# Performance work log

Measured on AMD Instinct MI355X. Metric: run time of the kernel, lower is better.

Reference implementation:

```python
import jax, jax.numpy as jnp
import numpy as np

D_MODEL = 1024
NUM_ATOMS = 16384
TEMPERATURE = 1.0
NEG_INF = -1e9


def setup_inputs() -> dict:
    key = jax.random.key(0)
    kx, kd, km = jax.random.split(key, 3)
    x = jax.random.normal(kx, (4, 2048, D_MODEL), dtype=jnp.float32)
    # xavier_uniform for [num_atoms, d_model]
    limit = float(np.sqrt(6.0 / (NUM_ATOMS + D_MODEL)))
    dictionary = jax.random.uniform(
        kd, (NUM_ATOMS, D_MODEL), dtype=jnp.float32, minval=-limit, maxval=limit
    )
    mask = jax.random.randint(km, (4, 2048, NUM_ATOMS), 0, 2, dtype=jnp.int32)
    return {"x": x, "dictionary": dictionary, "mask": mask}


def reference(x, dictionary, mask):
    # scores: [b, s, num_atoms]
    scores = jnp.einsum("bsd,ad->bsa", x, dictionary)
    m = mask.astype(scores.dtype)
    scores = scores * m + (1.0 - m) * NEG_INF
    weights = jax.nn.softmax(scores / TEMPERATURE, axis=-1)
    reconstruction = jnp.einsum("bsa,ad->bsd", weights, dictionary)
    argmax_indices = jnp.argmax(scores, axis=-1)
    return reconstruction, argmax_indices
```

## Files before the change

kernel.cpp:

```cpp
#include <hip/hip_runtime.h>

#define NTOK   8192
#define DMODEL 1024
#define NATOM  16384

typedef _Float16 half8  __attribute__((ext_vector_type(8)));
typedef _Float16 half4_t __attribute__((ext_vector_type(4)));
typedef float    f32x4  __attribute__((ext_vector_type(4)));

#define GLOAD_LDS16(gsrc, ldst) \
  __builtin_amdgcn_global_load_lds((const __attribute__((address_space(1))) unsigned int*)(gsrc), \
                                   (__attribute__((address_space(3))) unsigned int*)(ldst), 16, 0, 0)

__global__ void cvt_f32_f16(const float* __restrict__ in, _Float16* __restrict__ out, int n4) {
  int i = blockIdx.x * 256 + threadIdx.x;
  if (i >= n4) return;
  float4 v = ((const float4*)in)[i];
  half4_t h;
  h[0] = (_Float16)v.x; h[1] = (_Float16)v.y; h[2] = (_Float16)v.z; h[3] = (_Float16)v.w;
  ((half4_t*)out)[i] = h;
}

__global__ void transpose_dict(const float* __restrict__ dict,
                               _Float16* __restrict__ Dh, _Float16* __restrict__ dT) {
  __shared__ _Float16 tile[64][68];
  int a0 = blockIdx.x * 64;
  int d0 = blockIdx.y * 64;
  int tid = threadIdx.x;
  int c = tid & 63;
  int r0 = tid >> 6;
  #pragma unroll
  for (int i = 0; i < 16; i++) {
    int r = r0 + i * 4;
    _Float16 h = (_Float16)dict[(size_t)(a0 + r) * DMODEL + d0 + c];
    tile[r][c] = h;
    Dh[(size_t)(a0 + r) * DMODEL + d0 + c] = h;
  }
  __syncthreads();
  #pragma unroll
  for (int i = 0; i < 16; i++) {
    int rd = r0 + i * 4;
    dT[(size_t)(d0 + rd) * NATOM + a0 + c] = tile[c][rd];
  }
}

__global__ void zero_lsum(float* __restrict__ lsum) {
  lsum[blockIdx.x * 256 + threadIdx.x] = 0.0f;
}

__device__ __forceinline__ void stage_ab(const _Float16* __restrict__ A,
                                         const _Float16* __restrict__ B,
                                         _Float16* As, _Float16* Bs,
                                         size_t arow0, size_t brow0, size_t ldk,
                                         int k0, int tid) {
  #pragma unroll
  for (int i = 0; i < 2; i++) {
    int L = tid + i * 256;
    int r = L >> 2, pc = L & 3;
    int c = pc ^ ((r >> 1) & 3);
    GLOAD_LDS16(A + (arow0 + r) * ldk + k0 + c * 8, As + (size_t)L * 8);
    GLOAD_LDS16(B + (brow0 + r) * ldk + k0 + c * 8, Bs + (size_t)L * 8);
  }
}

__launch_bounds__(256, 2)
__global__ void score_kernel(const _Float16* __restrict__ Xh,
                             const _Float16* __restrict__ Dh,
                             const int* __restrict__ mask,
                             _Float16* __restrict__ E,
                             float* __restrict__ lsum,
                             _Float16* __restrict__ Tmax) {
  __shared__ _Float16 lds[17408];
  const int tid  = threadIdx.x;
  const int lane = tid & 63;
  const int wave = tid >> 6;
  const int wm = wave >> 1, wn = wave & 1;
  const int m0 = blockIdx.y * 128;
  const int n0 = blockIdx.x * 128;

  const int frow = lane & 15;
  const int fkc  = lane >> 4;

  f32x4 acc[4][4] = {};

  stage_ab(Xh, Dh, lds, lds + 4096, m0, n0, DMODEL, 0, tid);
  int cur = 0;
  for (int it = 0; it < DMODEL / 32; ++it) {
    __syncthreads();
    if (it + 1 < DMODEL / 32)
      stage_ab(Xh, Dh, lds + (cur ^ 1) * 8192, lds + (cur ^ 1) * 8192 + 4096,
               m0, n0, DMODEL, (it + 1) * 32, tid);
    _Float16* As = lds + cur * 8192;
    _Float16* Bs = As + 4096;
    half8 af[4], bf[4];
    #pragma unroll
    for (int i = 0; i < 4; i++) {
      int ar = wm * 64 + i * 16 + frow;
      int br = wn * 64 + i * 16 + frow;
      af[i] = *(const half8*)&As[ar * 32 + (fkc ^ ((ar >> 1) & 3)) * 8];
      bf[i] = *(const half8*)&Bs[br * 32 + (fkc ^ ((br >> 1) & 3)) * 8];
    }
    #pragma unroll
    for (int i = 0; i < 4; i++)
      #pragma unroll
      for (int j = 0; j < 4; j++)
        acc[i][j] = __builtin_amdgcn_mfma_f32_16x16x32_f16(af[i], bf[j], acc[i][j], 0, 0, 0);
    cur ^= 1;
  }

  __syncthreads();
  const int cr = (lane >> 4) * 4;
  const int cc = lane & 15;
  #pragma unroll
  for (int i = 0; i < 4; i++) {
    #pragma unroll
    for (int j = 0; j < 4; j++) {
      #pragma unroll
      for (int r = 0; r < 4; r++) {
        int lr = wm * 64 + i * 16 + cr + r;
        int lc = wn * 64 + j * 16 + cc;
        int mk = mask[(size_t)(m0 + lr) * NATOM + (n0 + lc)];
        float e = mk ? __expf(acc[i][j][r]) : 0.0f;
        lds[lr * 136 + lc] = (_Float16)e;
      }
    }
  }
  __syncthreads();
  #pragma unroll
  for (int i = 0; i < 8; i++) {
    int chunk = i * 256 + tid;
    int r  = chunk >> 4;
    int c8 = (chunk & 15) * 8;
    *(half8*)&E[(size_t)(m0 + r) * NATOM + n0 + c8] = *(const half8*)&lds[r * 136 + c8];
  }
  {
    int r = tid >> 1, h = tid & 1;
    const _Float16* rowp = &lds[r * 136 + h * 64];
    float s = 0.0f, m = 0.0f;
    #pragma unroll
    for (int i = 0; i < 8; i++) {
      half8 v = *(const half8*)&rowp[i * 8];
      #pragma unroll
      for (int j = 0; j < 8; j++) { float f = (float)v[j]; s += f; m = fmaxf(m, f); }
    }
    s += __shfl_xor(s, 1, 64);
    m = fmaxf(m, __shfl_xor(m, 1, 64));
    if (h == 0) {
      atomicAdd(&lsum[m0 + r], s);
      Tmax[(size_t)blockIdx.x * NTOK + m0 + r] = (_Float16)m;
    }
  }
}

__global__ void scan_lite(const _Float16* __restrict__ E,
                          const _Float16* __restrict__ Tmax,
                          const float* __restrict__ x,
                          const float* __restrict__ dict,
                          float* __restrict__ argout) {
  const int t = blockIdx.x;
  const int lane = threadIdx.x;
  float m0 = (float)Tmax[(size_t)lane * NTOK + t];
  float m1 = (float)Tmax[(size_t)(64 + lane) * NTOK + t];
  float mx = fmaxf(m0, m1);
  #pragma unroll
  for (int off = 32; off > 0; off >>= 1) mx = fmaxf(mx, __shfl_xor(mx, off, 64));

  __shared__ int cnt;
  __shared__ int cand[32];
  __shared__ double csc[32];
  if (lane == 0) cnt = 0;
  __syncthreads();

  if (mx > 0.0f) {
    float thr = 0.98f * mx;
    unsigned long long q0 = __ballot(m0 >= thr);
    unsigned long long q1 = __ballot(m1 >= thr);
    while (q0 | q1) {
      int tile;
      if (q0) { tile = __ffsll(q0) - 1; q0 &= q0 - 1; }
      else    { tile = 64 + __ffsll(q1) - 1; q1 &= q1 - 1; }
      const _Float16* ep = E + (size_t)t * NATOM + tile * 128;
      float e0 = (float)ep[lane], e1 = (float)ep[64 + lane];
      if (e0 >= thr) { int p = atomicAdd(&cnt, 1); if (p < 32) cand[p] = tile * 128 + lane; }
      if (e1 >= thr) { int p = atomicAdd(&cnt, 1); if (p < 32) cand[p] = tile * 128 + 64 + lane; }
    }
  }
  __syncthreads();
  int nc = min(cnt, 32);
  const float* xr = x + (size_t)t * DMODEL;
  for (int c = 0; c < nc; c++) {
    const float* dr = dict + (size_t)cand[c] * DMODEL;
    double a = 0.0;
    #pragma unroll
    for (int i = 0; i < 16; i++) {
      int d = lane + i * 64;
      a += (double)xr[d] * (double)dr[d];
    }
    #pragma unroll
    for (int off = 32; off > 0; off >>= 1) a += __shfl_down(a, off, 64);
    if (lane == 0) csc[c] = a;
  }
  __syncthreads();
  if (lane == 0) {
    int best = 0;
    if (nc > 0) {
      double bs = -1e300;
      best = NATOM;
      for (int c = 0; c < nc; c++)
        if (csc[c] > bs || (csc[c] == bs && cand[c] < best)) { bs = csc[c]; best = cand[c]; }
    }
    argout[t] = (float)best;
  }
}

__launch_bounds__(256, 2)
__global__ void recon_kernel(const _Float16* __restrict__ E,
                             const _Float16* __restrict__ DT,
                             const float* __restrict__ lsum,
                             float* __restrict__ out) {
  __shared__ _Float16 lds[20480];
  const int tid  = threadIdx.x;
  const int lane = tid & 63;
  const int wave = tid >> 6;
  const int m0 = blockIdx.y * 64;
  const int n0 = blockIdx.x * 256;

  const int frow = lane & 15;
  const int fkc  = lane >> 4;

  f32x4 acc[4][4] = {};

  auto stage = [&](int k0, int b) {
    _Float16* As = lds + b * 10240;
    _Float16* Bs = As + 2048;
    {
      int L = tid;
      int r = L >> 2, pc = L & 3;
      int c = pc ^ ((r >> 1) & 3);
      GLOAD_LDS16(E + (size_t)(m0 + r) * NATOM + k0 + c * 8, As + (size_t)L * 8);
    }
    #pragma unroll
    for (int i = 0; i < 4; i++) {
      int L = tid + i * 256;
      int r = L >> 2, pc = L & 3;
      int c = pc ^ ((r >> 1) & 3);
      GLOAD_LDS16(DT + (size_t)(n0 + r) * NATOM + k0 + c * 8, Bs + (size_t)L * 8);
    }
  };

  stage(0, 0);
  int cur = 0;
  for (int it = 0; it < NATOM / 32; ++it) {
    __syncthreads();
    if (it + 1 < NATOM / 32) stage((it + 1) * 32, cur ^ 1);
    _Float16* As = lds + cur * 10240;
    _Float16* Bs = As + 2048;
    half8 af[4], bf[4];
    #pragma unroll
    for (int i = 0; i < 4; i++) {
      int ar = i * 16 + frow;
      int br = wave * 64 + i * 16 + frow;
      af[i] = *(const half8*)&As[ar * 32 + (fkc ^ ((ar >> 1) & 3)) * 8];
      bf[i] = *(const half8*)&Bs[br * 32 + (fkc ^ ((br >> 1) & 3)) * 8];
    }
    #pragma unroll
    for (int i = 0; i < 4; i++)
      #pragma unroll
      for (int j = 0; j < 4; j++)
        acc[i][j] = __builtin_amdgcn_mfma_f32_16x16x32_f16(af[i], bf[j], acc[i][j], 0, 0, 0);
    cur ^= 1;
  }

  const int cr = (lane >> 4) * 4;
  const int cc = lane & 15;
  #pragma unroll
  for (int i = 0; i < 4; i++) {
    #pragma unroll
    for (int r = 0; r < 4; r++) {
      int lr = i * 16 + cr + r;
      float sc = 1.0f / lsum[m0 + lr];
      #pragma unroll
      for (int j = 0; j < 4; j++) {
        int lc = wave * 64 + j * 16 + cc;
        out[(size_t)(m0 + lr) * DMODEL + (n0 + lc)] = acc[i][j][r] * sc;
      }
    }
  }
}

extern "C" void kernel_launch(void* const* d_in, const int* in_sizes, int n_in,
                              void* d_out, int out_size, void* d_ws, size_t ws_size,
                              hipStream_t stream) {
  const float* x    = (const float*)d_in[0];
  const float* dict = (const float*)d_in[1];
  const int*   mask = (const int*)d_in[2];
  float* recon  = (float*)d_out;
  float* argout = recon + (size_t)NTOK * DMODEL;

  char* w = (char*)d_ws;
  _Float16* Xh = (_Float16*)(w);
  _Float16* Dh = (_Float16*)(w + (size_t)16  * 1024 * 1024);
  _Float16* DT = (_Float16*)(w + (size_t)48  * 1024 * 1024);
  _Float16* E  = (_Float16*)(w + (size_t)80  * 1024 * 1024);
  float*  lsum = (float*)  (w + (size_t)336 * 1024 * 1024);
  _Float16* Tmax = (_Float16*)d_out;

  cvt_f32_f16<<<dim3(NTOK * DMODEL / 4 / 256), 256, 0, stream>>>(x, Xh, NTOK * DMODEL / 4);
  transpose_dict<<<dim3(NATOM / 64, DMODEL / 64), 256, 0, stream>>>(dict, Dh, DT);
  zero_lsum<<<dim3(NTOK / 256), 256, 0, stream>>>(lsum);
  score_kernel<<<dim3(NATOM / 128, NTOK / 128), 256, 0, stream>>>(Xh, Dh, mask, E, lsum, Tmax);
  scan_lite<<<dim3(NTOK), 64, 0, stream>>>(E, Tmax, x, dict, argout);
  recon_kernel<<<dim3(DMODEL / 256, NTOK / 64), 256, 0, stream>>>(E, DT, lsum, recon);
}
```

Before: 1.494 ms.

## Prefetch mask bits during score GEMM and split-K the recon GEMM

In the score kernel, the int32 mask is now read in coalesced int4 chunks spread across the K loop iterations and packed into bitmasks in LDS. The epilogue then reads bits from LDS instead of doing scattered global mask loads, which should hide mask latency behind the MFMA work. The recon GEMM is split into two K halves over blockIdx.z, writing partial sums to the output and a workspace buffer (reusing the Xh region). A new combine kernel adds the halves and applies the 1/lsum normalization. Launch bounds are also raised to 4 blocks per SM, which risks register spilling.

```diff
diff --git a/kernel.cpp b/kernel.cpp
--- a/kernel.cpp
+++ b/kernel.cpp
@@ -63,14 +63,15 @@
   }
 }
 
-__launch_bounds__(256, 2)
+__launch_bounds__(256, 4)
 __global__ void score_kernel(const _Float16* __restrict__ Xh,
                              const _Float16* __restrict__ Dh,
                              const int* __restrict__ mask,
                              _Float16* __restrict__ E,
                              float* __restrict__ lsum,
                              _Float16* __restrict__ Tmax) {
-  __shared__ _Float16 lds[17408];
+  __shared__ _Float16 lds[18432];
+  char* ldsM = (char*)(lds + 17408);
   const int tid  = threadIdx.x;
   const int lane = tid & 63;
   const int wave = tid >> 6;
@@ -81,15 +82,28 @@
   const int frow = lane & 15;
   const int fkc  = lane >> 4;
 
+  const int mr = tid >> 1, mh = tid & 1;
+  const int* mrow = mask + (size_t)(m0 + mr) * NATOM + n0 + mh * 64;
+
   f32x4 acc[4][4] = {};
+  int4 mv;
+  unsigned int mbits = 0;
 
   stage_ab(Xh, Dh, lds, lds + 4096, m0, n0, DMODEL, 0, tid);
   int cur = 0;
-  for (int it = 0; it < DMODEL / 32; ++it) {
+  auto kstep = [&](int it, int phase) {
     __syncthreads();
     if (it + 1 < DMODEL / 32)
       stage_ab(Xh, Dh, lds + (cur ^ 1) * 8192, lds + (cur ^ 1) * 8192 + 4096,
                m0, n0, DMODEL, (it + 1) * 32, tid);
+    if (phase == 0) mv = *(const int4*)(mrow + (it >> 1) * 4);
+    else if (phase == 1)
+      mbits = (mv.x != 0) | ((mv.y != 0) << 1) | ((mv.z != 0) << 2) | ((mv.w != 0) << 3);
+    else if (phase == 2) mv = *(const int4*)(mrow + (it >> 1) * 4);
+    else {
+      mbits |= ((mv.x != 0) << 4) | ((mv.y != 0) << 5) | ((mv.z != 0) << 6) | ((mv.w != 0) << 7);
+      ldsM[mr * 16 + mh * 8 + (it >> 2)] = (char)mbits;
+    }
     _Float16* As = lds + cur * 8192;
     _Float16* Bs = As + 4096;
     half8 af[4], bf[4];
@@ -106,6 +120,10 @@
       for (int j = 0; j < 4; j++)
         acc[i][j] = __builtin_amdgcn_mfma_f32_16x16x32_f16(af[i], bf[j], acc[i][j], 0, 0, 0);
     cur ^= 1;
+  };
+  for (int it4 = 0; it4 < 8; ++it4) {
+    kstep(it4 * 4 + 0, 0); kstep(it4 * 4 + 1, 1);
+    kstep(it4 * 4 + 2, 2); kstep(it4 * 4 + 3, 3);
   }
 
   __syncthreads();
@@ -113,13 +131,17 @@
   const int cc = lane & 15;
   #pragma unroll
   for (int i = 0; i < 4; i++) {
+    unsigned long long rb[4];
+    #pragma unroll
+    for (int r = 0; r < 4; r++)
+      rb[r] = *(const unsigned long long*)&ldsM[(wm * 64 + i * 16 + cr + r) * 16 + wn * 8];
     #pragma unroll
     for (int j = 0; j < 4; j++) {
       #pragma unroll
       for (int r = 0; r < 4; r++) {
         int lr = wm * 64 + i * 16 + cr + r;
         int lc = wn * 64 + j * 16 + cc;
-        int mk = mask[(size_t)(m0 + lr) * NATOM + (n0 + lc)];
+        unsigned int mk = (unsigned int)(rb[r] >> (j * 16 + cc)) & 1u;
         float e = mk ? __expf(acc[i][j][r]) : 0.0f;
         lds[lr * 136 + lc] = (_Float16)e;
       }
@@ -213,17 +235,18 @@
   }
 }
 
-__launch_bounds__(256, 2)
+__launch_bounds__(256, 4)
 __global__ void recon_kernel(const _Float16* __restrict__ E,
                              const _Float16* __restrict__ DT,
-                             const float* __restrict__ lsum,
-                             float* __restrict__ out) {
+                             float* __restrict__ out,
+                             float* __restrict__ P1) {
   __shared__ _Float16 lds[20480];
   const int tid  = threadIdx.x;
   const int lane = tid & 63;
   const int wave = tid >> 6;
   const int m0 = blockIdx.y * 64;
   const int n0 = blockIdx.x * 256;
+  const int kbase = blockIdx.z * (NATOM / 2);
 
   const int frow = lane & 15;
   const int fkc  = lane >> 4;
@@ -248,11 +271,12 @@
     }
   };
 
-  stage(0, 0);
+  stage(kbase, 0);
   int cur = 0;
-  for (int it = 0; it < NATOM / 32; ++it) {
+  const int NIT = (NATOM / 2) / 32;
+  for (int it = 0; it < NIT; ++it) {
     __syncthreads();
-    if (it + 1 < NATOM / 32) stage((it + 1) * 32, cur ^ 1);
+    if (it + 1 < NIT) stage(kbase + (it + 1) * 32, cur ^ 1);
     _Float16* As = lds + cur * 10240;
     _Float16* Bs = As + 2048;
     half8 af[4], bf[4];
@@ -271,6 +295,7 @@
     cur ^= 1;
   }
 
+  float* P = blockIdx.z ? P1 : out;
   const int cr = (lane >> 4) * 4;
   const int cc = lane & 15;
   #pragma unroll
@@ -278,14 +303,26 @@
     #pragma unroll
     for (int r = 0; r < 4; r++) {
       int lr = i * 16 + cr + r;
-      float sc = 1.0f / lsum[m0 + lr];
       #pragma unroll
       for (int j = 0; j < 4; j++) {
         int lc = wave * 64 + j * 16 + cc;
-        out[(size_t)(m0 + lr) * DMODEL + (n0 + lc)] = acc[i][j][r] * sc;
+        P[(size_t)(m0 + lr) * DMODEL + (n0 + lc)] = acc[i][j][r];
       }
     }
   }
+}
+
+__global__ void combine_kernel(float* __restrict__ out, const float* __restrict__ P1,
+                               const float* __restrict__ lsum) {
+  int t = blockIdx.x;
+  int d = threadIdx.x;
+  float inv = 1.0f / lsum[t];
+  float4* o = (float4*)(out + (size_t)t * DMODEL);
+  const float4* p = (const float4*)(P1 + (size_t)t * DMODEL);
+  float4 a = o[d], b = p[d];
+  a.x = (a.x + b.x) * inv; a.y = (a.y + b.y) * inv;
+  a.z = (a.z + b.z) * inv; a.w = (a.w + b.w) * inv;
+  o[d] = a;
 }
 
 extern "C" void kernel_launch(void* const* d_in, const int* in_sizes, int n_in,
@@ -303,6 +340,7 @@
   _Float16* DT = (_Float16*)(w + (size_t)48  * 1024 * 1024);
   _Float16* E  = (_Float16*)(w + (size_t)80  * 1024 * 1024);
   float*  lsum = (float*)  (w + (size_t)336 * 1024 * 1024);
+  float*  P1   = (float*)w;
   _Float16* Tmax = (_Float16*)d_out;
 
   cvt_f32_f16<<<dim3(NTOK * DMODEL / 4 / 256), 256, 0, stream>>>(x, Xh, NTOK * DMODEL / 4);
@@ -310,5 +348,6 @@
   zero_lsum<<<dim3(NTOK / 256), 256, 0, stream>>>(lsum);
   score_kernel<<<dim3(NATOM / 128, NTOK / 128), 256, 0, stream>>>(Xh, Dh, mask, E, lsum, Tmax);
   scan_lite<<<dim3(NTOK), 64, 0, stream>>>(E, Tmax, x, dict, argout);
-  recon_kernel<<<dim3(DMODEL / 256, NTOK / 64), 256, 0, stream>>>(E, DT, lsum, recon);
-}
+  recon_kernel<<<dim3(DMODEL / 256, NTOK / 64, 2), 256, 0, stream>>>(E, DT, recon, P1);
+  combine_kernel<<<dim3(NTOK), 256, 0, stream>>>(recon, P1, lsum);
+}
```

Measured after the change: 1.717 ms. 14.9% more time.
